# Kernel tuning notes

Measured on AMD Instinct MI355X. Metric: run time of the kernel, lower is better.

The kernel has to match this reference:

```python
import jax, jax.numpy as jnp
import numpy as np

B, L = 256, 50            # batch, n_pos (session length)
ITEM_DIM, POS_DIM = 128, 64
DIM = ITEM_DIM + POS_DIM  # 192
N_ITEMS = 50000
W = 20.0                  # temperature / init scale
LN_EPS = 1e-5


def renorm(t, max_norm=1.5):
    # torch Embedding max_norm semantics: clip row L2 norm to max_norm
    n = jnp.linalg.norm(t, axis=-1, keepdims=True)
    return t * jnp.minimum(1.0, max_norm / jnp.maximum(n, 1e-7))


def setup_inputs() -> dict:
    key = jax.random.key(0)
    ks = jax.random.split(key, 24)
    inv_w = 1.0 / W
    lb = 1.0 / np.sqrt(DIM)
    lb3 = 1.0 / np.sqrt(3 * DIM)
    u = lambda k, shape, b: jax.random.uniform(k, shape, jnp.float32, -b, b)
    emb = jax.random.normal(ks[0], (N_ITEMS, ITEM_DIM), jnp.float32).at[0].set(0.0)
    pos_emb = jax.random.normal(ks[1], (L + 1, POS_DIM), jnp.float32).at[0].set(0.0)
    return {
        'x': jax.random.randint(ks[20], (B, L), 0, N_ITEMS),
        'pos': jnp.sort(jax.random.randint(ks[21], (B, L), 1, L + 1), axis=-1),
        'emb': emb,
        'pos_emb': pos_emb,
        'vw0': jax.random.normal(ks[2], (1, DIM), jnp.float32) * inv_w,
        'vw1': jax.random.normal(ks[3], (DIM, DIM), jnp.float32) * inv_w,
        'vw2': jax.random.normal(ks[4], (DIM, DIM), jnp.float32) * inv_w,
        'vbias': jnp.zeros((DIM,), jnp.float32),
        'w1_W': u(ks[5], (DIM, DIM), lb), 'w1_b': u(ks[6], (DIM,), lb),
        'w2_W': u(ks[7], (DIM, DIM), lb), 'w2_b': u(ks[8], (DIM,), lb),
        'wA': jax.random.normal(ks[9], (1, L), jnp.float32) * inv_w,
        'wg1_W': u(ks[10], (DIM, DIM), lb), 'wg1_b': u(ks[11], (DIM,), lb),
        'wg2_W': u(ks[12], (DIM, DIM), lb), 'wg2_b': u(ks[13], (DIM,), lb),
        'gq': jax.random.normal(ks[14], (DIM, 1), jnp.float32) * inv_w,
        'wf_W': u(ks[15], (ITEM_DIM, 3 * DIM), lb3), 'wf_b': u(ks[16], (ITEM_DIM,), lb3),
        'ln_g': jnp.ones((DIM,), jnp.float32), 'ln_b': jnp.zeros((DIM,), jnp.float32),
    }


def reference(x, pos, emb, pos_emb, vw0, vw1, vw2, vbias, w1_W, w1_b, w2_W, w2_b,
              wA, wg1_W, wg1_b, wg2_W, wg2_b, gq, wf_W, wf_b, ln_g, ln_b):
    emb_r = renorm(emb)
    x_e = emb_r[x]                                   # [B,L,item_dim]
    p_e = renorm(pos_emb)[pos]                       # [B,L,pos_dim]
    x_ = jnp.concatenate([x_e, p_e], axis=-1)        # [B,L,D]
    mask = (x != 0)                                  # [B,L]

    # --- vanila (additive) attention, all n_pos targets in one fused pass ---
    K = x_ @ vw1                                     # [B,L,D]  (shared across targets)
    Q = x_ @ vw2                                     # [B,L,D]
    h = jax.nn.relu(K[:, None, :, :] + Q[:, :, None, :] + vbias)   # [B,Li,Lj,D]
    alpha = jnp.einsum('bijd,d->bij', h, vw0[0])     # scores over keys j
    alpha = jnp.where(mask[:, None, :], alpha, -jnp.inf)
    a = jax.nn.softmax(alpha, axis=-1)
    S = jnp.einsum('bij,bjd->bid', a, x_)            # [B,L,D]

    # --- MLP + LayerNorm + position mixing ---
    h2 = jax.nn.relu(S @ w1_W.T + w1_b)
    S2 = h2 @ w2_W.T + w2_b + S
    mu = jnp.mean(S2, axis=-1, keepdims=True)
    var = jnp.mean((S2 - mu) ** 2, axis=-1, keepdims=True)
    S3 = ln_g * (S2 - mu) * jax.lax.rsqrt(var + LN_EPS) + ln_b
    st = jnp.einsum('p,bpd->bd', wA[0], S3)[:, None, :]   # [B,1,D]

    # --- global attention ---
    sl = x_[:, -1:, :]                               # [B,1,D]
    g = jax.nn.sigmoid(x_ @ wg1_W.T + wg1_b + (sl @ wg2_W.T + wg2_b))
    ag = g @ gq                                      # [B,L,1]
    sg = jnp.einsum('blo,bld->bod', ag, x_)          # [B,1,D]

    # --- decoder: cosine-similarity logits against item embeddings ---
    c = jax.nn.selu(jnp.concatenate([st, sl, sg], axis=-1) @ wf_W.T + wf_b)[:, 0, :]
    c = c / jnp.linalg.norm(c, axis=-1, keepdims=True)
    le = emb_r[1:]
    le = le / jnp.linalg.norm(le, axis=-1, keepdims=True)
    z = W * (c @ le.T)                               # [B, n_items-1]
    return z
```

## Files before the change

### kernel.cpp

```cpp
#include <hip/hip_runtime.h>
#include <hip/hip_bf16.h>
#include <math.h>
#include <stdint.h>

#define BB 256
#define LL 50
#define IDIM 128
#define PDIM 64
#define DIM 192
#define NITEMS 50000
#define NOUT 49999
#define WSC 20.0f
#define EPS 1e-5f
#define WMAT (DIM * DIM)

typedef __attribute__((ext_vector_type(8))) short  short8;
typedef __attribute__((ext_vector_type(4))) float  f32x4;

__device__ __forceinline__ unsigned short f2bf(float f) {
    unsigned int u = __float_as_uint(f);
    u = (u + 0x7FFFu + ((u >> 16) & 1u)) >> 16;
    return (unsigned short)u;
}
__device__ __forceinline__ float bf2f(unsigned short u) {
    unsigned int v = ((unsigned int)u) << 16;
    return __uint_as_float(v);
}

__global__ __launch_bounds__(256) void k_prep(const float* __restrict__ emb,
                                              float* __restrict__ scale,
                                              float* __restrict__ invn,
                                              unsigned short* __restrict__ emb16,
                                              const float* __restrict__ pe,
                                              float* __restrict__ pscale,
                                              const float* __restrict__ vw1, const float* __restrict__ vw2,
                                              const float* __restrict__ w1W, const float* __restrict__ w2W,
                                              const float* __restrict__ wg1W,
                                              unsigned short* __restrict__ Wout) {
    int blk = blockIdx.x;
    if (blk < 12500) {
        int row  = blk * 4 + (threadIdx.x >> 6);
        int lane = threadIdx.x & 63;
        const float* p = emb + (size_t)row * IDIM;
        float a = p[lane], b = p[lane + 64];
        emb16[(size_t)row * IDIM + lane]      = f2bf(a);
        emb16[(size_t)row * IDIM + lane + 64] = f2bf(b);
        float s = a * a + b * b;
#pragma unroll
        for (int off = 32; off; off >>= 1) s += __shfl_xor(s, off);
        if (lane == 0) {
            float n = sqrtf(s);
            scale[row] = fminf(1.0f, 1.5f / fmaxf(n, 1e-7f));
            invn[row]  = (n > 0.f) ? 1.f / n : 0.f;
        }
    } else if (blk < 12500 + 720) {
        int b = blk - 12500;
        int wi = b / 144;
        int pos = (b % 144) * 256 + threadIdx.x;
        int n = pos / DIM, k = pos - n * DIM;
        float v;
        if      (wi == 0) v = vw1[(size_t)k * DIM + n];
        else if (wi == 1) v = vw2[(size_t)k * DIM + n];
        else if (wi == 2) v = w1W[pos];
        else if (wi == 3) v = w2W[pos];
        else              v = wg1W[pos];
        Wout[(size_t)wi * WMAT + pos] = f2bf(v);
    } else {
        int row = threadIdx.x;
        if (row <= LL) {
            float s = 0.f;
            const float* p = pe + row * PDIM;
            for (int d = 0; d < PDIM; ++d) { float v = p[d]; s += v * v; }
            float n = sqrtf(s);
            pscale[row] = fminf(1.0f, 1.5f / fmaxf(n, 1e-7f));
        }
    }
}

__global__ __launch_bounds__(768, 3) void k_mega(
    const int* __restrict__ x, const int* __restrict__ pos,
    const float* __restrict__ emb, const float* __restrict__ pe,
    const float* __restrict__ scale, const float* __restrict__ pscale,
    const unsigned short* __restrict__ W16,
    const float* __restrict__ vw0, const float* __restrict__ vbias,
    const float* __restrict__ w1b, const float* __restrict__ w2b,
    const float* __restrict__ wg1b, const float* __restrict__ wg2W,
    const float* __restrict__ wg2b, const float* __restrict__ gq,
    const float* __restrict__ wA, const float* __restrict__ lng,
    const float* __restrict__ lnb, const float* __restrict__ wfW,
    const float* __restrict__ wfb, unsigned short* __restrict__ Cb16g) {

    __shared__ unsigned short Bs16[64 * DIM];
    __shared__ unsigned short X16T[DIM * 72];
    __shared__ unsigned short Ab16[64 * 72];
    __shared__ float R1[LL * 196];
    __shared__ float R2[LL * 196];
    __shared__ float xlast[DIM];
    __shared__ float GLs[DIM];
    __shared__ float cvec[3 * DIM];
    __shared__ float stB[DIM], sgB[DIM];
    __shared__ float red2[6][128];
    __shared__ float ags[64];
    __shared__ int   msk[64];
    __shared__ float was[64];
    __shared__ float red[12];
    __shared__ int   xi[LL], pii[LL];
    __shared__ float xsc[LL], psc[LL];

    const int b = blockIdx.x, t = threadIdx.x;
    const int wv = t >> 6, l = t & 63;
    const int lr = l & 15, lk = l >> 4;

    if (t < LL) {
        int v = x[b * LL + t];  xi[t] = v;  xsc[t] = scale[v];
        int pv = pos[b * LL + t]; pii[t] = pv; psc[t] = pscale[pv];
    }
    if (t >= 64 && t < 128) ags[t - 64] = 0.f;
    if (t >= 128 && t < 128 + LL) was[t - 128] = wA[t - 128];
    __syncthreads();
    if (t < 64) msk[t] = (t < LL) ? xi[t] : 0;
    for (int r = wv; r < LL; r += 12) {
        float sx = xsc[r], sp = psc[r];
        float v0 = emb[(size_t)xi[r] * IDIM + l] * sx;
        float v1 = emb[(size_t)xi[r] * IDIM + l + 64] * sx;
        float v2 = pe[pii[r] * PDIM + l] * sp;
        int base = r * 384, sw = (r & 7) << 4;
        *(unsigned short*)((char*)Bs16 + ((base + l * 2) ^ sw))         = f2bf(v0);
        *(unsigned short*)((char*)Bs16 + ((base + (l + 64) * 2) ^ sw))  = f2bf(v1);
        *(unsigned short*)((char*)Bs16 + ((base + (l + 128) * 2) ^ sw)) = f2bf(v2);
        X16T[l * 72 + r]         = f2bf(v0);
        X16T[(l + 64) * 72 + r]  = f2bf(v1);
        X16T[(l + 128) * 72 + r] = f2bf(v2);
        if (r == 49) { xlast[l] = v0; xlast[l + 64] = v1; xlast[l + 128] = v2; }
    }
    for (int e = t; e < 14 * DIM; e += 768) Bs16[LL * DIM + e] = 0;
    for (int e = t; e < DIM * 14; e += 768) { int d = e / 14, j = 50 + (e - d * 14); X16T[d * 72 + j] = 0; }
    for (int e = t; e < 14 * 72; e += 768) Ab16[50 * 72 + e] = 0;
    __syncthreads();

    if (t < DIM) {
        float g = wg2b[t];
        const float* wr = wg2W + (size_t)t * DIM;
        float s0 = 0, s1 = 0, s2 = 0, s3 = 0;
        for (int k = 0; k < DIM; k += 4) {
            float4 w4 = *(const float4*)(wr + k);
            s0 += xlast[k] * w4.x; s1 += xlast[k + 1] * w4.y;
            s2 += xlast[k + 2] * w4.z; s3 += xlast[k + 3] * w4.w;
        }
        GLs[t] = g + ((s0 + s1) + (s2 + s3));
    }
    __syncthreads();

    for (int task = wv; task < 36; task += 12) {
        int out = task / 12, nt = task % 12;
        int ncol = nt * 16 + lr;
        const unsigned short* bp = W16 + (size_t)(out == 0 ? 0 : (out == 1 ? 1 : 4)) * WMAT
                                   + (size_t)ncol * DIM + lk * 8;
#pragma unroll
        for (int mt = 0; mt < 4; ++mt) {
            int row = mt * 16 + lr;
            f32x4 ac = {};
#pragma unroll
            for (int ks = 0; ks < 6; ++ks) {
                int byte = (row * 384 + (lk * 8 + ks * 32) * 2) ^ ((row & 7) << 4);
                short8 af = *(const short8*)((const char*)Bs16 + byte);
                short8 bf = *(const short8*)(bp + ks * 32);
                ac = __builtin_amdgcn_mfma_f32_16x16x32_bf16(af, bf, ac, 0, 0, 0);
            }
            if (out == 0) {
                float bia = vbias[ncol];
#pragma unroll
                for (int r = 0; r < 4; ++r) {
                    int gr = mt * 16 + lk * 4 + r;
                    if (gr < LL) R1[gr * 196 + ncol] = ac[r] + bia;
                }
            } else if (out == 1) {
#pragma unroll
                for (int r = 0; r < 4; ++r) {
                    int gr = mt * 16 + lk * 4 + r;
                    if (gr < LL) R2[gr * 196 + ncol] = ac[r];
                }
            } else {
                float bia = wg1b[ncol] + GLs[ncol];
                float gqv = gq[ncol];
                int gr0 = mt * 16 + lk * 4;
                float v0 = ac[0] + bia, v1 = ac[1] + bia, v2 = ac[2] + bia, v3 = ac[3] + bia;
                float c0 = (gr0 + 0 < LL) ? gqv / (1.f + expf(-v0)) : 0.f;
                float c1 = (gr0 + 1 < LL) ? gqv / (1.f + expf(-v1)) : 0.f;
                float c2 = (gr0 + 2 < LL) ? gqv / (1.f + expf(-v2)) : 0.f;
                float c3 = (gr0 + 3 < LL) ? gqv / (1.f + expf(-v3)) : 0.f;
#pragma unroll
                for (int off = 1; off < 16; off <<= 1) {
                    c0 += __shfl_xor(c0, off); c1 += __shfl_xor(c1, off);
                    c2 += __shfl_xor(c2, off); c3 += __shfl_xor(c3, off);
                }
                if (lr == 0) {
                    if (gr0 + 0 < LL) atomicAdd(&ags[gr0 + 0], c0);
                    if (gr0 + 1 < LL) atomicAdd(&ags[gr0 + 1], c1);
                    if (gr0 + 2 < LL) atomicAdd(&ags[gr0 + 2], c2);
                    if (gr0 + 3 < LL) atomicAdd(&ags[gr0 + 3], c3);
                }
            }
        }
    }
    __syncthreads();

    {
        const int d0 = wv * 16;
        float kr[16], wr[16];
        {
            const float* wp = vw0 + d0;
#pragma unroll
            for (int q = 0; q < 4; ++q) {
                float4 v = *(const float4*)(wp + q * 4);
                wr[q * 4] = v.x; wr[q * 4 + 1] = v.y; wr[q * 4 + 2] = v.z; wr[q * 4 + 3] = v.w;
            }
            if (l < LL) {
                const float* kp = R1 + l * 196 + d0;
#pragma unroll
                for (int q = 0; q < 4; ++q) {
                    float4 v = *(const float4*)(kp + q * 4);
                    kr[q * 4] = v.x; kr[q * 4 + 1] = v.y; kr[q * 4 + 2] = v.z; kr[q * 4 + 3] = v.w;
                }
            } else {
#pragma unroll
                for (int q = 0; q < 16; ++q) kr[q] = 0.f;
            }
        }
        __syncthreads();
        unsigned short* parts16 = (unsigned short*)R1;
        const float NEG = -__builtin_inff();
        bool valid = (l < LL) && (msk[l] != 0);
#pragma unroll
        for (int i0 = 0; i0 < LL; i0 += 25) {
            for (int i = 0; i < 25; ++i) {
                const float* qrow = R2 + (i0 + i) * 196 + d0;
                float b0 = 0, b1 = 0, b2 = 0, b3 = 0;
#pragma unroll
                for (int q = 0; q < 4; ++q) {
                    float4 qv = *(const float4*)(qrow + q * 4);
                    b0 += fmaxf(kr[q * 4 + 0] + qv.x, 0.f) * wr[q * 4 + 0];
                    b1 += fmaxf(kr[q * 4 + 1] + qv.y, 0.f) * wr[q * 4 + 1];
                    b2 += fmaxf(kr[q * 4 + 2] + qv.z, 0.f) * wr[q * 4 + 2];
                    b3 += fmaxf(kr[q * 4 + 3] + qv.w, 0.f) * wr[q * 4 + 3];
                }
                parts16[(wv * 25 + i) * 64 + l] = f2bf((b0 + b1) + (b2 + b3));
            }
            __syncthreads();
            for (int i = wv; i < 25; i += 12) {
                float aj = 0.f;
#pragma unroll
                for (int w2 = 0; w2 < 12; ++w2) aj += bf2f(parts16[(w2 * 25 + i) * 64 + l]);
                if (!valid) aj = NEG;
                float m = aj;
#pragma unroll
                for (int off = 32; off; off >>= 1) m = fmaxf(m, __shfl_xor(m, off));
                float e = valid ? expf(aj - m) : 0.f;
                float s = e;
#pragma unroll
                for (int off = 32; off; off >>= 1) s += __shfl_xor(s, off);
                Ab16[(i0 + i) * 72 + l] = f2bf(e / s);
            }
            __syncthreads();
        }
    }

    for (int task = wv; task < 48; task += 12) {
        int mt = task / 12, nt = task - (task / 12) * 12;
        int i0 = mt * 16, d0c = nt * 16;
        short8 aA0 = *(const short8*)(Ab16 + (i0 + lr) * 72 + lk * 8);
        short8 aA1 = *(const short8*)(Ab16 + (i0 + lr) * 72 + 32 + lk * 8);
        short8 bB0 = *(const short8*)(X16T + (d0c + lr) * 72 + lk * 8);
        short8 bB1 = *(const short8*)(X16T + (d0c + lr) * 72 + 32 + lk * 8);
        f32x4 ac = {};
        ac = __builtin_amdgcn_mfma_f32_16x16x32_bf16(aA0, bB0, ac, 0, 0, 0);
        ac = __builtin_amdgcn_mfma_f32_16x16x32_bf16(aA1, bB1, ac, 0, 0, 0);
        int d = d0c + lr;
#pragma unroll
        for (int r = 0; r < 4; ++r) {
            int i = i0 + lk * 4 + r;
            if (i < LL) {
                R2[i * 196 + d] = ac[r];
                int byte = (i * 384 + d * 2) ^ ((i & 7) << 4);
                *(unsigned short*)((char*)Bs16 + byte) = f2bf(ac[r]);
            }
        }
    }
    __syncthreads();

    {
        f32x4 h[4] = {};
        {
            int ncol = wv * 16 + lr;
            const unsigned short* bp = W16 + (size_t)2 * WMAT + (size_t)ncol * DIM + lk * 8;
#pragma unroll
            for (int mt = 0; mt < 4; ++mt) {
                int row = mt * 16 + lr;
#pragma unroll
                for (int ks = 0; ks < 6; ++ks) {
                    int byte = (row * 384 + (lk * 8 + ks * 32) * 2) ^ ((row & 7) << 4);
                    short8 sf = *(const short8*)((const char*)Bs16 + byte);
                    short8 bf = *(const short8*)(bp + ks * 32);
                    h[mt] = __builtin_amdgcn_mfma_f32_16x16x32_bf16(sf, bf, h[mt], 0, 0, 0);
                }
            }
        }
        __syncthreads();
        {
            int gc = wv * 16 + lr;
            float bia = w1b[gc];
#pragma unroll
            for (int mt = 0; mt < 4; ++mt)
#pragma unroll
                for (int r = 0; r < 4; ++r) {
                    int gr = mt * 16 + lk * 4 + r;
                    if (gr < LL) {
                        float v = fmaxf(h[mt][r] + bia, 0.f);
                        int byte = (gr * 384 + gc * 2) ^ ((gr & 7) << 4);
                        *(unsigned short*)((char*)Bs16 + byte) = f2bf(v);
                    }
                }
        }
    }
    __syncthreads();

    {
        int ncol = wv * 16 + lr;
        const unsigned short* bp = W16 + (size_t)3 * WMAT + (size_t)ncol * DIM + lk * 8;
        float bia = w2b[ncol];
#pragma unroll
        for (int mt = 0; mt < 4; ++mt) {
            int row = mt * 16 + lr;
            f32x4 ac = {};
#pragma unroll
            for (int ks = 0; ks < 6; ++ks) {
                int byte = (row * 384 + (lk * 8 + ks * 32) * 2) ^ ((row & 7) << 4);
                short8 hf = *(const short8*)((const char*)Bs16 + byte);
                short8 bf = *(const short8*)(bp + ks * 32);
                ac = __builtin_amdgcn_mfma_f32_16x16x32_bf16(hf, bf, ac, 0, 0, 0);
            }
#pragma unroll
            for (int r = 0; r < 4; ++r) {
                int gr = mt * 16 + lk * 4 + r;
                if (gr < LL) R2[gr * 196 + ncol] = ac[r] + bia + R2[gr * 196 + ncol];
            }
        }
    }
    __syncthreads();

    for (int r = wv; r < LL; r += 12) {
        float* p = R2 + r * 196;
        float v0 = p[l], v1 = p[l + 64], v2 = p[l + 128];
        float s = v0 + v1 + v2;
#pragma unroll
        for (int off = 32; off; off >>= 1) s += __shfl_xor(s, off);
        float mu = s * (1.f / DIM);
        float d0 = v0 - mu, d1 = v1 - mu, d2 = v2 - mu;
        float q = d0 * d0 + d1 * d1 + d2 * d2;
#pragma unroll
        for (int off = 32; off; off >>= 1) q += __shfl_xor(q, off);
        float inv = rsqrtf(q * (1.f / DIM) + EPS);
        p[l]       = lng[l] * d0 * inv + lnb[l];
        p[l + 64]  = lng[l + 64] * d1 * inv + lnb[l + 64];
        p[l + 128] = lng[l + 128] * d2 * inv + lnb[l + 128];
    }
    __syncthreads();

    if (t < DIM) {
        float st = 0.f;
        for (int p = 0; p < 25; ++p) st += was[p] * R2[p * 196 + t];
        cvec[t] = st;
        cvec[DIM + t] = xlast[t];
    } else if (t < 2 * DIM) {
        int d = t - DIM;
        float st = 0.f;
        for (int p = 25; p < LL; ++p) st += was[p] * R2[p * 196 + d];
        stB[d] = st;
    } else if (t < 3 * DIM) {
        int d = t - 2 * DIM;
        float sg = 0.f;
        const unsigned short* xr = X16T + d * 72;
        for (int p = 0; p < 25; ++p) sg += ags[p] * bf2f(xr[p]);
        cvec[2 * DIM + d] = sg;
    } else {
        int d = t - 3 * DIM;
        float sg = 0.f;
        const unsigned short* xr = X16T + d * 72;
        for (int p = 25; p < LL; ++p) sg += ags[p] * bf2f(xr[p]);
        sgB[d] = sg;
    }
    __syncthreads();
    if (t < DIM) {
        cvec[t] += stB[t];
        cvec[2 * DIM + t] += sgB[t];
    }
    __syncthreads();

    {
        int out = t & 127, part = t >> 7;
        float s = (part == 0) ? wfb[out] : 0.f;
        const float* wr = wfW + (size_t)out * (3 * DIM) + part * 96;
        const float* cv = cvec + part * 96;
        for (int e = 0; e < 96; e += 4) {
            float4 w4 = *(const float4*)(wr + e);
            s += cv[e] * w4.x + cv[e + 1] * w4.y + cv[e + 2] * w4.z + cv[e + 3] * w4.w;
        }
        red2[part][out] = s;
    }
    __syncthreads();
    float cj = 0.f;
    if (t < IDIM) {
        float s = red2[0][t] + red2[1][t] + red2[2][t]
                + red2[3][t] + red2[4][t] + red2[5][t];
        const float sa = 1.6732632423543772f, sc = 1.0507009873554805f;
        cj = sc * (s > 0.f ? s : sa * expm1f(s));
    }
    float sq = cj * cj;
#pragma unroll
    for (int off = 32; off; off >>= 1) sq += __shfl_xor(sq, off);
    if (l == 0 && wv < 2) red[wv] = sq;
    __syncthreads();
    if (t < IDIM) {
        float nrm = sqrtf(red[0] + red[1]);
        Cb16g[b * IDIM + t] = f2bf(cj / nrm);
    }
}

__global__ __launch_bounds__(256) void k_z4(const unsigned short* __restrict__ Cb16,
                                            const unsigned short* __restrict__ emb16,
                                            const float* __restrict__ invn,
                                            float* __restrict__ Z) {
    __shared__ float tr[4][64][68];
    int n0 = blockIdx.x * 64;
    int t = threadIdx.x, w = t >> 6, l = t & 63;
    int lr = l & 15, lk = l >> 4;

    short8 a[4][4];
#pragma unroll
    for (int mt = 0; mt < 4; ++mt) {
        int mrow = w * 64 + mt * 16 + lr;
        const unsigned short* ap = Cb16 + (size_t)mrow * IDIM + lk * 8;
#pragma unroll
        for (int ks = 0; ks < 4; ++ks) a[mt][ks] = *(const short8*)(ap + ks * 32);
    }
    f32x4 acc[4][4] = {};
#pragma unroll
    for (int nt = 0; nt < 4; ++nt) {
        int nrow = n0 + nt * 16 + lr;
        short8 bfr[4];
        if (nrow < NOUT) {
            const unsigned short* bp = emb16 + (size_t)(nrow + 1) * IDIM + lk * 8;
#pragma unroll
            for (int ks = 0; ks < 4; ++ks) bfr[ks] = *(const short8*)(bp + ks * 32);
        } else {
            short8 z = {};
#pragma unroll
            for (int ks = 0; ks < 4; ++ks) bfr[ks] = z;
        }
#pragma unroll
        for (int mt = 0; mt < 4; ++mt)
#pragma unroll
            for (int ks = 0; ks < 4; ++ks)
                acc[mt][nt] = __builtin_amdgcn_mfma_f32_16x16x32_bf16(a[mt][ks], bfr[ks], acc[mt][nt], 0, 0, 0);
    }
#pragma unroll
    for (int nt = 0; nt < 4; ++nt) {
        int gn = n0 + nt * 16 + lr;
        float sc = (gn < NOUT) ? WSC * invn[gn + 1] : 0.f;
#pragma unroll
        for (int mt = 0; mt < 4; ++mt)
#pragma unroll
            for (int r = 0; r < 4; ++r)
                tr[w][mt * 16 + lk * 4 + r][nt * 16 + lr] = acc[mt][nt][r] * sc;
    }
    __syncthreads();
    int q = l >> 4, s = l & 15;
    bool tail = (n0 + 64) > NOUT;
#pragma unroll
    for (int it = 0; it < 16; ++it) {
        int row = it * 4 + q;
        int gm  = w * 64 + row;
        float4 v = *(const float4*)&tr[w][row][s * 4];
        if (!tail) {
            *(float4*)&Z[(size_t)gm * NOUT + n0 + s * 4] = v;
        } else {
            int c0 = n0 + s * 4;
            float vv[4] = {v.x, v.y, v.z, v.w};
#pragma unroll
            for (int j = 0; j < 4; ++j)
                if (c0 + j < NOUT) Z[(size_t)gm * NOUT + c0 + j] = vv[j];
        }
    }
}

extern "C" void kernel_launch(void* const* d_in, const int* in_sizes, int n_in,
                              void* d_out, int out_size, void* d_ws, size_t ws_size,
                              hipStream_t stream) {
    const int*   x     = (const int*)d_in[0];
    const int*   pos   = (const int*)d_in[1];
    const float* emb   = (const float*)d_in[2];
    const float* pose  = (const float*)d_in[3];
    const float* vw0   = (const float*)d_in[4];
    const float* vw1   = (const float*)d_in[5];
    const float* vw2   = (const float*)d_in[6];
    const float* vbias = (const float*)d_in[7];
    const float* w1W   = (const float*)d_in[8];
    const float* w1b   = (const float*)d_in[9];
    const float* w2W   = (const float*)d_in[10];
    const float* w2b   = (const float*)d_in[11];
    const float* wA    = (const float*)d_in[12];
    const float* wg1W  = (const float*)d_in[13];
    const float* wg1b  = (const float*)d_in[14];
    const float* wg2W  = (const float*)d_in[15];
    const float* wg2b  = (const float*)d_in[16];
    const float* gq    = (const float*)d_in[17];
    const float* wfW   = (const float*)d_in[18];
    const float* wfb   = (const float*)d_in[19];
    const float* lng   = (const float*)d_in[20];
    const float* lnb   = (const float*)d_in[21];
    float* Z = (float*)d_out;

    float* w = (float*)d_ws;
    float* scale  = w; w += NITEMS;
    float* invn   = w; w += NITEMS;
    float* pscale = w; w += 64;
    w = (float*)(((uintptr_t)w + 15) & ~(uintptr_t)15);
    unsigned short* emb16 = (unsigned short*)w; w += (size_t)NITEMS * IDIM / 2;
    unsigned short* W16   = (unsigned short*)w; w += (size_t)5 * WMAT / 2;
    unsigned short* Cb16  = (unsigned short*)w; w += (size_t)BB * IDIM / 2;

    k_prep<<<12500 + 720 + 1, 256, 0, stream>>>(emb, scale, invn, emb16, pose, pscale,
                                                vw1, vw2, w1W, w2W, wg1W, W16);
    k_mega<<<BB, 768, 0, stream>>>(x, pos, emb, pose, scale, pscale, W16,
                                   vw0, vbias, w1b, w2b, wg1b, wg2W, wg2b, gq,
                                   wA, lng, lnb, wfW, wfb, Cb16);
    k_z4<<<(NOUT + 63) / 64, 256, 0, stream>>>(Cb16, emb16, invn, Z);
}
```

Baseline: 101.0 us.

## Remove prep kernel by fusing renorm, bf16 conversion and norms into consumers

Drops the separate prep pass that converted the embedding table and weight matrices to bf16 and precomputed row norms. The main kernel now computes renorm scales for gathered rows with wave shuffles and converts fp32 weights to bf16 fragments on the fly. The logits kernel reads fp32 embeddings directly and computes row norms in-register. This removes a full pass over the 50000x128 table and one launch, at the cost of reading fp32 (twice the bytes) in the logits GEMM and redundant weight conversion in every block, including strided column reads for the transposed vw1/vw2.

After: 129.9 us. 1.29x slower.

```diff
diff --git a/kernel.cpp b/kernel.cpp
--- a/kernel.cpp
+++ b/kernel.cpp
@@ -12,9 +12,9 @@
 #define NOUT 49999
 #define WSC 20.0f
 #define EPS 1e-5f
-#define WMAT (DIM * DIM)
 
 typedef __attribute__((ext_vector_type(8))) short  short8;
+typedef __attribute__((ext_vector_type(8))) unsigned short u16x8;
 typedef __attribute__((ext_vector_type(4))) float  f32x4;
 
 __device__ __forceinline__ unsigned short f2bf(float f) {
@@ -26,62 +26,19 @@
     unsigned int v = ((unsigned int)u) << 16;
     return __uint_as_float(v);
 }
-
-__global__ __launch_bounds__(256) void k_prep(const float* __restrict__ emb,
-                                              float* __restrict__ scale,
-                                              float* __restrict__ invn,
-                                              unsigned short* __restrict__ emb16,
-                                              const float* __restrict__ pe,
-                                              float* __restrict__ pscale,
-                                              const float* __restrict__ vw1, const float* __restrict__ vw2,
-                                              const float* __restrict__ w1W, const float* __restrict__ w2W,
-                                              const float* __restrict__ wg1W,
-                                              unsigned short* __restrict__ Wout) {
-    int blk = blockIdx.x;
-    if (blk < 12500) {
-        int row  = blk * 4 + (threadIdx.x >> 6);
-        int lane = threadIdx.x & 63;
-        const float* p = emb + (size_t)row * IDIM;
-        float a = p[lane], b = p[lane + 64];
-        emb16[(size_t)row * IDIM + lane]      = f2bf(a);
-        emb16[(size_t)row * IDIM + lane + 64] = f2bf(b);
-        float s = a * a + b * b;
-#pragma unroll
-        for (int off = 32; off; off >>= 1) s += __shfl_xor(s, off);
-        if (lane == 0) {
-            float n = sqrtf(s);
-            scale[row] = fminf(1.0f, 1.5f / fmaxf(n, 1e-7f));
-            invn[row]  = (n > 0.f) ? 1.f / n : 0.f;
-        }
-    } else if (blk < 12500 + 720) {
-        int b = blk - 12500;
-        int wi = b / 144;
-        int pos = (b % 144) * 256 + threadIdx.x;
-        int n = pos / DIM, k = pos - n * DIM;
-        float v;
-        if      (wi == 0) v = vw1[(size_t)k * DIM + n];
-        else if (wi == 1) v = vw2[(size_t)k * DIM + n];
-        else if (wi == 2) v = w1W[pos];
-        else if (wi == 3) v = w2W[pos];
-        else              v = wg1W[pos];
-        Wout[(size_t)wi * WMAT + pos] = f2bf(v);
-    } else {
-        int row = threadIdx.x;
-        if (row <= LL) {
-            float s = 0.f;
-            const float* p = pe + row * PDIM;
-            for (int d = 0; d < PDIM; ++d) { float v = p[d]; s += v * v; }
-            float n = sqrtf(s);
-            pscale[row] = fminf(1.0f, 1.5f / fmaxf(n, 1e-7f));
-        }
-    }
+__device__ __forceinline__ short8 pack8(const float* v) {
+    u16x8 o;
+#pragma unroll
+    for (int j = 0; j < 8; ++j) o[j] = f2bf(v[j]);
+    return *(short8*)&o;
 }
 
 __global__ __launch_bounds__(768, 3) void k_mega(
     const int* __restrict__ x, const int* __restrict__ pos,
     const float* __restrict__ emb, const float* __restrict__ pe,
-    const float* __restrict__ scale, const float* __restrict__ pscale,
-    const unsigned short* __restrict__ W16,
+    const float* __restrict__ vw1, const float* __restrict__ vw2,
+    const float* __restrict__ w1W, const float* __restrict__ w2W,
+    const float* __restrict__ wg1W,
     const float* __restrict__ vw0, const float* __restrict__ vbias,
     const float* __restrict__ w1b, const float* __restrict__ w2b,
     const float* __restrict__ wg1b, const float* __restrict__ wg2W,
@@ -105,25 +62,34 @@
     __shared__ float was[64];
     __shared__ float red[12];
     __shared__ int   xi[LL], pii[LL];
-    __shared__ float xsc[LL], psc[LL];
 
     const int b = blockIdx.x, t = threadIdx.x;
     const int wv = t >> 6, l = t & 63;
     const int lr = l & 15, lk = l >> 4;
 
     if (t < LL) {
-        int v = x[b * LL + t];  xi[t] = v;  xsc[t] = scale[v];
-        int pv = pos[b * LL + t]; pii[t] = pv; psc[t] = pscale[pv];
+        xi[t]  = x[b * LL + t];
+        pii[t] = pos[b * LL + t];
     }
     if (t >= 64 && t < 128) ags[t - 64] = 0.f;
     if (t >= 128 && t < 128 + LL) was[t - 128] = wA[t - 128];
     __syncthreads();
     if (t < 64) msk[t] = (t < LL) ? xi[t] : 0;
     for (int r = wv; r < LL; r += 12) {
-        float sx = xsc[r], sp = psc[r];
-        float v0 = emb[(size_t)xi[r] * IDIM + l] * sx;
-        float v1 = emb[(size_t)xi[r] * IDIM + l + 64] * sx;
-        float v2 = pe[pii[r] * PDIM + l] * sp;
+        float v0 = emb[(size_t)xi[r] * IDIM + l];
+        float v1 = emb[(size_t)xi[r] * IDIM + l + 64];
+        float v2 = pe[pii[r] * PDIM + l];
+        float se = v0 * v0 + v1 * v1;
+        float sp = v2 * v2;
+#pragma unroll
+        for (int off = 32; off; off >>= 1) {
+            se += __shfl_xor(se, off);
+            sp += __shfl_xor(sp, off);
+        }
+        float ne = sqrtf(se), np = sqrtf(sp);
+        float sce = fminf(1.0f, 1.5f / fmaxf(ne, 1e-7f));
+        float scp = fminf(1.0f, 1.5f / fmaxf(np, 1e-7f));
+        v0 *= sce; v1 *= sce; v2 *= scp;
         int base = r * 384, sw = (r & 7) << 4;
         *(unsigned short*)((char*)Bs16 + ((base + l * 2) ^ sw))         = f2bf(v0);
         *(unsigned short*)((char*)Bs16 + ((base + (l + 64) * 2) ^ sw))  = f2bf(v1);
@@ -154,8 +120,29 @@
     for (int task = wv; task < 36; task += 12) {
         int out = task / 12, nt = task % 12;
         int ncol = nt * 16 + lr;
-        const unsigned short* bp = W16 + (size_t)(out == 0 ? 0 : (out == 1 ? 1 : 4)) * WMAT
-                                   + (size_t)ncol * DIM + lk * 8;
+        short8 wb[6];
+        if (out < 2) {
+            const float* Wm = (out == 0) ? vw1 : vw2;
+#pragma unroll
+            for (int ks = 0; ks < 6; ++ks) {
+                float tmp[8];
+#pragma unroll
+                for (int j = 0; j < 8; ++j)
+                    tmp[j] = Wm[(size_t)(ks * 32 + lk * 8 + j) * DIM + ncol];
+                wb[ks] = pack8(tmp);
+            }
+        } else {
+            const float* Wm = wg1W + (size_t)ncol * DIM + lk * 8;
+#pragma unroll
+            for (int ks = 0; ks < 6; ++ks) {
+                float tmp[8];
+                float4 a4 = *(const float4*)(Wm + ks * 32);
+                float4 b4 = *(const float4*)(Wm + ks * 32 + 4);
+                tmp[0] = a4.x; tmp[1] = a4.y; tmp[2] = a4.z; tmp[3] = a4.w;
+                tmp[4] = b4.x; tmp[5] = b4.y; tmp[6] = b4.z; tmp[7] = b4.w;
+                wb[ks] = pack8(tmp);
+            }
+        }
 #pragma unroll
         for (int mt = 0; mt < 4; ++mt) {
             int row = mt * 16 + lr;
@@ -164,8 +151,7 @@
             for (int ks = 0; ks < 6; ++ks) {
                 int byte = (row * 384 + (lk * 8 + ks * 32) * 2) ^ ((row & 7) << 4);
                 short8 af = *(const short8*)((const char*)Bs16 + byte);
-                short8 bf = *(const short8*)(bp + ks * 32);
-                ac = __builtin_amdgcn_mfma_f32_16x16x32_bf16(af, bf, ac, 0, 0, 0);
+                ac = __builtin_amdgcn_mfma_f32_16x16x32_bf16(af, wb[ks], ac, 0, 0, 0);
             }
             if (out == 0) {
                 float bia = vbias[ncol];
@@ -290,9 +276,19 @@
 
     {
         f32x4 h[4] = {};
+        short8 wb[6];
         {
             int ncol = wv * 16 + lr;
-            const unsigned short* bp = W16 + (size_t)2 * WMAT + (size_t)ncol * DIM + lk * 8;
+            const float* Wm = w1W + (size_t)ncol * DIM + lk * 8;
+#pragma unroll
+            for (int ks = 0; ks < 6; ++ks) {
+                float tmp[8];
+                float4 a4 = *(const float4*)(Wm + ks * 32);
+                float4 b4 = *(const float4*)(Wm + ks * 32 + 4);
+                tmp[0] = a4.x; tmp[1] = a4.y; tmp[2] = a4.z; tmp[3] = a4.w;
+                tmp[4] = b4.x; tmp[5] = b4.y; tmp[6] = b4.z; tmp[7] = b4.w;
+                wb[ks] = pack8(tmp);
+            }
 #pragma unroll
             for (int mt = 0; mt < 4; ++mt) {
                 int row = mt * 16 + lr;
@@ -300,8 +296,7 @@
                 for (int ks = 0; ks < 6; ++ks) {
                     int byte = (row * 384 + (lk * 8 + ks * 32) * 2) ^ ((row & 7) << 4);
                     short8 sf = *(const short8*)((const char*)Bs16 + byte);
-                    short8 bf = *(const short8*)(bp + ks * 32);
-                    h[mt] = __builtin_amdgcn_mfma_f32_16x16x32_bf16(sf, bf, h[mt], 0, 0, 0);
+                    h[mt] = __builtin_amdgcn_mfma_f32_16x16x32_bf16(sf, wb[ks], h[mt], 0, 0, 0);
                 }
             }
         }
@@ -326,7 +321,17 @@
 
     {
         int ncol = wv * 16 + lr;
-        const unsigned short* bp = W16 + (size_t)3 * WMAT + (size_t)ncol * DIM + lk * 8;
+        short8 wb[6];
+        const float* Wm = w2W + (size_t)ncol * DIM + lk * 8;
+#pragma unroll
+        for (int ks = 0; ks < 6; ++ks) {
+            float tmp[8];
+            float4 a4 = *(const float4*)(Wm + ks * 32);
+            float4 b4 = *(const float4*)(Wm + ks * 32 + 4);
+            tmp[0] = a4.x; tmp[1] = a4.y; tmp[2] = a4.z; tmp[3] = a4.w;
+            tmp[4] = b4.x; tmp[5] = b4.y; tmp[6] = b4.z; tmp[7] = b4.w;
+            wb[ks] = pack8(tmp);
+        }
         float bia = w2b[ncol];
 #pragma unroll
         for (int mt = 0; mt < 4; ++mt) {
@@ -336,8 +341,7 @@
             for (int ks = 0; ks < 6; ++ks) {
                 int byte = (row * 384 + (lk * 8 + ks * 32) * 2) ^ ((row & 7) << 4);
                 short8 hf = *(const short8*)((const char*)Bs16 + byte);
-                short8 bf = *(const short8*)(bp + ks * 32);
-                ac = __builtin_amdgcn_mfma_f32_16x16x32_bf16(hf, bf, ac, 0, 0, 0);
+                ac = __builtin_amdgcn_mfma_f32_16x16x32_bf16(hf, wb[ks], ac, 0, 0, 0);
             }
 #pragma unroll
             for (int r = 0; r < 4; ++r) {
@@ -426,9 +430,8 @@
     }
 }
 
-__global__ __launch_bounds__(256) void k_z4(const unsigned short* __restrict__ Cb16,
-                                            const unsigned short* __restrict__ emb16,
-                                            const float* __restrict__ invn,
+__global__ __launch_bounds__(256) void k_z5(const unsigned short* __restrict__ Cb16,
+                                            const float* __restrict__ emb,
                                             float* __restrict__ Z) {
     __shared__ float tr[4][64][68];
     int n0 = blockIdx.x * 64;
@@ -444,19 +447,34 @@
         for (int ks = 0; ks < 4; ++ks) a[mt][ks] = *(const short8*)(ap + ks * 32);
     }
     f32x4 acc[4][4] = {};
+    float sc[4];
 #pragma unroll
     for (int nt = 0; nt < 4; ++nt) {
         int nrow = n0 + nt * 16 + lr;
         short8 bfr[4];
+        float ssq = 0.f;
         if (nrow < NOUT) {
-            const unsigned short* bp = emb16 + (size_t)(nrow + 1) * IDIM + lk * 8;
-#pragma unroll
-            for (int ks = 0; ks < 4; ++ks) bfr[ks] = *(const short8*)(bp + ks * 32);
+            const float* bp = emb + (size_t)(nrow + 1) * IDIM + lk * 8;
+#pragma unroll
+            for (int ks = 0; ks < 4; ++ks) {
+                float tmp[8];
+                float4 a4 = *(const float4*)(bp + ks * 32);
+                float4 b4 = *(const float4*)(bp + ks * 32 + 4);
+                tmp[0] = a4.x; tmp[1] = a4.y; tmp[2] = a4.z; tmp[3] = a4.w;
+                tmp[4] = b4.x; tmp[5] = b4.y; tmp[6] = b4.z; tmp[7] = b4.w;
+#pragma unroll
+                for (int j = 0; j < 8; ++j) ssq += tmp[j] * tmp[j];
+                bfr[ks] = pack8(tmp);
+            }
         } else {
             short8 z = {};
 #pragma unroll
             for (int ks = 0; ks < 4; ++ks) bfr[ks] = z;
         }
+        ssq += __shfl_xor(ssq, 16);
+        ssq += __shfl_xor(ssq, 32);
+        float n = sqrtf(ssq);
+        sc[nt] = (nrow < NOUT && n > 0.f) ? WSC / n : 0.f;
 #pragma unroll
         for (int mt = 0; mt < 4; ++mt)
 #pragma unroll
@@ -465,13 +483,11 @@
     }
 #pragma unroll
     for (int nt = 0; nt < 4; ++nt) {
-        int gn = n0 + nt * 16 + lr;
-        float sc = (gn < NOUT) ? WSC * invn[gn + 1] : 0.f;
 #pragma unroll
         for (int mt = 0; mt < 4; ++mt)
 #pragma unroll
             for (int r = 0; r < 4; ++r)
-                tr[w][mt * 16 + lk * 4 + r][nt * 16 + lr] = acc[mt][nt][r] * sc;
+                tr[w][mt * 16 + lk * 4 + r][nt * 16 + lr] = acc[mt][nt][r] * sc[nt];
     }
     __syncthreads();
     int q = l >> 4, s = l & 15;
@@ -521,18 +537,12 @@
     float* Z = (float*)d_out;
 
     float* w = (float*)d_ws;
-    float* scale  = w; w += NITEMS;
-    float* invn   = w; w += NITEMS;
-    float* pscale = w; w += 64;
     w = (float*)(((uintptr_t)w + 15) & ~(uintptr_t)15);
-    unsigned short* emb16 = (unsigned short*)w; w += (size_t)NITEMS * IDIM / 2;
-    unsigned short* W16   = (unsigned short*)w; w += (size_t)5 * WMAT / 2;
-    unsigned short* Cb16  = (unsigned short*)w; w += (size_t)BB * IDIM / 2;
-
-    k_prep<<<12500 + 720 + 1, 256, 0, stream>>>(emb, scale, invn, emb16, pose, pscale,
-                                                vw1, vw2, w1W, w2W, wg1W, W16);
-    k_mega<<<BB, 768, 0, stream>>>(x, pos, emb, pose, scale, pscale, W16,
+    unsigned short* Cb16 = (unsigned short*)w;
+
+    k_mega<<<BB, 768, 0, stream>>>(x, pos, emb, pose,
+                                   vw1, vw2, w1W, w2W, wg1W,
                                    vw0, vbias, w1b, w2b, wg1b, wg2W, wg2b, gq,
                                    wA, lng, lnb, wfW, wfb, Cb16);
-    k_z4<<<(NOUT + 63) / 64, 256, 0, stream>>>(Cb16, emb16, invn, Z);
+    k_z5<<<(NOUT + 63) / 64, 256, 0, stream>>>(Cb16, emb, Z);
 }
```
